# Kernel tuning notes

Hardware: AMD Instinct MI355X
Metric: run time of the kernel (lower is better)

## Reference

```python
import jax, jax.numpy as jnp
import numpy as np

N_NODES = 100000
N_EDGES = 1600000


def setup_inputs() -> dict:
    key = jax.random.key(0)
    ks = jax.random.split(key, 8)
    s = 0.1  # small init scale
    return {
        "x": jax.random.normal(ks[0], (N_NODES, 58), jnp.float32),
        "edge_index": jax.random.randint(ks[1], (2, N_EDGES), 0, N_NODES, dtype=jnp.int32),
        "Wi1": s * jax.random.normal(ks[2], (2, 58, 16), jnp.float32),
        "Wr1": s * jax.random.normal(ks[3], (2, 58, 16), jnp.float32),
        "b1": s * jax.random.normal(ks[4], (2, 16), jnp.float32),
        "Wi2": s * jax.random.normal(ks[5], (2, 16, 1), jnp.float32),
        "Wr2": s * jax.random.normal(ks[6], (2, 16, 1), jnp.float32),
        "b2": s * jax.random.normal(ks[7], (2, 1), jnp.float32),
    }


def _gcn_norm(edge_index, n_nodes):
    # PyG gcn_norm with add_self_loops=False: deg from target col, sym norm
    row, col = edge_index[0], edge_index[1]
    deg = jax.ops.segment_sum(jnp.ones((edge_index.shape[1],), jnp.float32), col,
                              num_segments=n_nodes)
    dis = jnp.where(deg > 0, jax.lax.rsqrt(jnp.maximum(deg, 1.0)), 0.0)
    return row, col, dis[row] * dis[col]  # per-edge norm


def _arma_layer(x, row, col, norm, Wi, Wr, b, n_nodes):
    # T=1, shared_weights, eval-mode (internal dropout off):
    # out_k = relu(A_hat @ (x @ Wi_k) + x @ Wr_k + b_k); mean over K stacks
    h = jnp.einsum('nf,kfo->kno', x, Wi)          # [K, N, F_out]
    msg = h[:, row, :] * norm[None, :, None]      # [K, E, F_out]
    agg = jax.vmap(lambda m: jax.ops.segment_sum(m, col, num_segments=n_nodes))(msg)
    root = jnp.einsum('nf,kfo->kno', x, Wr)       # [K, N, F_out]
    return jax.nn.relu(agg + root + b[:, None, :]).mean(axis=0)


def reference(x, edge_index, Wi1, Wr1, b1, Wi2, Wr2, b2):
    row, col, norm = _gcn_norm(edge_index, N_NODES)
    h = _arma_layer(x, row, col, norm, Wi1, Wr1, b1, N_NODES)  # conv1 (relu inside)
    h = jax.nn.relu(h)                                         # wrapper F.relu
    # F.dropout(p=0.5) is identity in eval mode
    out = _arma_layer(h, row, col, norm, Wi2, Wr2, b2, N_NODES)  # conv2
    return out  # [N, 1]
```

## Files before the change

kernel.cpp:

```cpp
#include <hip/hip_runtime.h>

#define NN 100000
#define NE 1600000

constexpr int F_IN = 58;
constexpr int FH2  = 32;
constexpr int KS   = 2;

constexpr int NB   = 391;
constexpr int NBLK = 256;
constexpr int EPB  = NE / NBLK;
constexpr int SCANN = NB * NBLK;
constexpr int SCAN_BLOCKS = (SCANN + 1023) / 1024;
constexpr int DN_NODES = 64;
constexpr int DENSE_BLOCKS = (NN + DN_NODES - 1) / DN_NODES;
constexpr int LROW = 136;

using short8 = __attribute__((ext_vector_type(8))) short;
using f32x4  = __attribute__((ext_vector_type(4))) float;

__device__ inline void splitbf(float v, short& hi, short& lo) {
    unsigned ub = __float_as_uint(v);
    unsigned short h = (unsigned short)(ub >> 16);
    float hif = __uint_as_float(((unsigned)h) << 16);
    float lof = v - hif;
    unsigned short l = (unsigned short)(__float_as_uint(lof) >> 16);
    hi = (short)h; lo = (short)l;
}

__device__ inline unsigned short bf16rne(float v) {
    unsigned u = __float_as_uint(v);
    unsigned r = u + 0x7FFF + ((u >> 16) & 1);
    return (unsigned short)(r >> 16);
}

__device__ inline float bf2f(unsigned short s) {
    return __uint_as_float(((unsigned)s) << 16);
}

__global__ void k_prep_w(const float* __restrict__ Wi, const float* __restrict__ Wr,
                         short* __restrict__ wpre) {
    int t = threadIdx.x;
    for (int idx = t; idx < 64 * 64; idx += 256) {
        int c = idx >> 6, i = idx & 63;
        int ko = c & 31, kst = ko >> 4, o = ko & 15;
        const float* W = (c < 32) ? Wi : Wr;
        float v = (i < F_IN) ? W[(kst * F_IN + i) * 16 + o] : 0.f;
        short hi, lo; splitbf(v, hi, lo);
        wpre[c * 128 + i] = hi;
        wpre[c * 128 + 64 + i] = lo;
    }
}

__global__ void k_hist_dense1(const int* __restrict__ col, int* __restrict__ bh,
                              const float* __restrict__ x,
                              const short* __restrict__ wpre,
                              const float* __restrict__ b,
                              unsigned short* __restrict__ h1b,
                              unsigned short* __restrict__ r1b) {
    __shared__ int hist[NB];
    __shared__ short sA[64 * LROW];
    __shared__ short sB[64 * LROW];
    int tid = threadIdx.x;

    if (blockIdx.x < NBLK) {
        int blk = blockIdx.x;
        for (int i = tid; i < NB; i += 256) hist[i] = 0;
        __syncthreads();
        const int2* c2p = (const int2*)&col[blk * EPB];
        for (int c = tid; c < EPB / 2; c += 256) {
            int2 cc = c2p[c];
            atomicAdd(&hist[cc.x >> 8], 1);
            atomicAdd(&hist[cc.y >> 8], 1);
        }
        __syncthreads();
        for (int i = tid; i < NB; i += 256)
            bh[i * NBLK + blk] = hist[i];
        return;
    }

    int nodeBase = (blockIdx.x - NBLK) * DN_NODES;
    for (int t = tid; t < 1024; t += 256) {
        int c = t >> 4, q8 = t & 15;
        *(short8*)&sB[c * LROW + q8 * 8] = *(const short8*)&wpre[c * 128 + q8 * 8];
    }
    for (int t = tid; t < 1024; t += 256) {
        int r = t >> 4, q4 = t & 15;
        int n = nodeBase + r;
        float v0 = 0.f, v1 = 0.f, v2 = 0.f, v3 = 0.f;
        int i0 = q4 * 4;
        if (n < NN && i0 < F_IN) {
            float2 a = *(const float2*)&x[(size_t)n * F_IN + i0];
            v0 = a.x; v1 = a.y;
            if (i0 + 2 < F_IN) {
                float2 c2 = *(const float2*)&x[(size_t)n * F_IN + i0 + 2];
                v2 = c2.x; v3 = c2.y;
            }
        }
        short h0, l0, h1s, l1s, h2s, l2s, h3s, l3s;
        splitbf(v0, h0, l0); splitbf(v1, h1s, l1s);
        splitbf(v2, h2s, l2s); splitbf(v3, h3s, l3s);
        *(short4*)&sA[r * LROW + q4 * 4]      = make_short4(h0, h1s, h2s, h3s);
        *(short4*)&sA[r * LROW + 64 + q4 * 4] = make_short4(l0, l1s, l2s, l3s);
    }
    __syncthreads();

    int lane = tid & 63, w = tid >> 6;
    int r15 = lane & 15, h4 = lane >> 4;
    const short* aB = &sA[(w * 16 + r15) * LROW];
    f32x4 acc0 = {0,0,0,0}, acc1 = {0,0,0,0}, acc2 = {0,0,0,0}, acc3 = {0,0,0,0};
    const int kaA[6] = {0, 32, 0, 32, 64, 96};
    const int kaB[6] = {0, 32, 64, 96, 0, 32};
#pragma unroll
    for (int s = 0; s < 6; s++) {
        short8 af = *(const short8*)&aB[kaA[s] + h4 * 8];
#define BMM(nt, accv) { \
        short8 bf = *(const short8*)&sB[(nt * 16 + r15) * LROW + kaB[s] + h4 * 8]; \
        accv = __builtin_amdgcn_mfma_f32_16x16x32_bf16(af, bf, accv, 0, 0, 0); }
        BMM(0, acc0) BMM(1, acc1) BMM(2, acc2) BMM(3, acc3)
#undef BMM
    }
    int nb0 = nodeBase + w * 16 + h4 * 4;
#define WH(nt, accv) { int colg = nt * 16 + r15; \
    if (nb0 + 0 < NN) h1b[(size_t)(nb0 + 0) * 32 + colg] = bf16rne(accv[0]); \
    if (nb0 + 1 < NN) h1b[(size_t)(nb0 + 1) * 32 + colg] = bf16rne(accv[1]); \
    if (nb0 + 2 < NN) h1b[(size_t)(nb0 + 2) * 32 + colg] = bf16rne(accv[2]); \
    if (nb0 + 3 < NN) h1b[(size_t)(nb0 + 3) * 32 + colg] = bf16rne(accv[3]); }
#define WR(nt, accv) { int colg = nt * 16 + r15 - 32; float bv = b[colg]; \
    if (nb0 + 0 < NN) r1b[(size_t)(nb0 + 0) * 32 + colg] = bf16rne(accv[0] + bv); \
    if (nb0 + 1 < NN) r1b[(size_t)(nb0 + 1) * 32 + colg] = bf16rne(accv[1] + bv); \
    if (nb0 + 2 < NN) r1b[(size_t)(nb0 + 2) * 32 + colg] = bf16rne(accv[2] + bv); \
    if (nb0 + 3 < NN) r1b[(size_t)(nb0 + 3) * 32 + colg] = bf16rne(accv[3] + bv); }
    WH(0, acc0) WH(1, acc1) WR(2, acc2) WR(3, acc3)
#undef WH
#undef WR
}

__global__ void k_scan1(int* __restrict__ bh, int* __restrict__ bsum) {
    __shared__ int ts[256];
    int tid = threadIdx.x;
    int base = blockIdx.x * 1024 + tid * 4;
    int v0 = (base + 0 < SCANN) ? bh[base + 0] : 0;
    int v1 = (base + 1 < SCANN) ? bh[base + 1] : 0;
    int v2 = (base + 2 < SCANN) ? bh[base + 2] : 0;
    int v3 = (base + 3 < SCANN) ? bh[base + 3] : 0;
    int p0 = v0, p1 = p0 + v1, p2 = p1 + v2, p3 = p2 + v3;
    ts[tid] = p3;
    __syncthreads();
    for (int off = 1; off < 256; off <<= 1) {
        int v = (tid >= off) ? ts[tid - off] : 0;
        __syncthreads();
        ts[tid] += v;
        __syncthreads();
    }
    int prev = (tid > 0) ? ts[tid - 1] : 0;
    if (base + 0 < SCANN) bh[base + 0] = prev + p0;
    if (base + 1 < SCANN) bh[base + 1] = prev + p1;
    if (base + 2 < SCANN) bh[base + 2] = prev + p2;
    if (base + 3 < SCANN) bh[base + 3] = prev + p3;
    if (tid == 255) bsum[blockIdx.x] = ts[255];
}

__global__ void k_scan2(const int* __restrict__ bsum, int* __restrict__ boff) {
    __shared__ int s[128];
    int tid = threadIdx.x;
    s[tid] = (tid < SCAN_BLOCKS) ? bsum[tid] : 0;
    __syncthreads();
    for (int off = 1; off < 128; off <<= 1) {
        int v = (tid >= off) ? s[tid - off] : 0;
        __syncthreads();
        s[tid] += v;
        __syncthreads();
    }
    if (tid < SCAN_BLOCKS) boff[tid] = (tid > 0) ? s[tid - 1] : 0;
}

__global__ void k_bscatter(const int* __restrict__ row, const int* __restrict__ col,
                           const int* __restrict__ bh, const int* __restrict__ boff,
                           int* __restrict__ ebuck) {
    __shared__ int cur[NB];
    int tid = threadIdx.x, blk = blockIdx.x;
    for (int i = tid; i < NB; i += 256) {
        int idx = i * NBLK + blk;
        cur[i] = (idx == 0) ? 0 : bh[idx - 1] + boff[(idx - 1) >> 10];
    }
    __syncthreads();
    int base = blk * EPB;
    const int2* c2p = (const int2*)&col[base];
    const int2* r2p = (const int2*)&row[base];
    for (int c = tid; c < EPB / 2; c += 256) {
        int2 cc = c2p[c];
        int2 rr = r2p[c];
        int p0 = atomicAdd(&cur[cc.x >> 8], 1);
        ebuck[p0] = (rr.x << 8) | (cc.x & 255);
        int p1 = atomicAdd(&cur[cc.y >> 8], 1);
        ebuck[p1] = (rr.y << 8) | (cc.y & 255);
    }
}

__global__ void __launch_bounds__(256) k_bcsr(const int* __restrict__ bh,
                                              const int* __restrict__ boff,
                                              const int* __restrict__ ebuck,
                                              int* __restrict__ inc, float* __restrict__ dis,
                                              int* __restrict__ esrc) {
    __shared__ int cnt[514];
    __shared__ int scn[256];
    __shared__ int cur[256];
    int b = blockIdx.x, tid = threadIdx.x;
    int i0 = b * NBLK - 1, i1 = (b + 1) * NBLK - 1;
    int start = (b == 0) ? 0 : bh[i0] + boff[i0 >> 10];
    int end   = bh[i1] + boff[i1 >> 10];
    cnt[tid] = 0; cnt[257 + tid] = 0;
    __syncthreads();
    int c0 = (tid & 1) * 257;
    for (int j = start + tid; j < end; j += 256)
        atomicAdd(&cnt[c0 + (ebuck[j] & 255)], 1);
    __syncthreads();
    int v = cnt[tid] + cnt[257 + tid];
    scn[tid] = v;
    __syncthreads();
    for (int off = 1; off < 256; off <<= 1) {
        int t = (tid >= off) ? scn[tid - off] : 0;
        __syncthreads();
        scn[tid] += t;
        __syncthreads();
    }
    int incl = scn[tid];
    cur[tid] = start + incl - v;
    int colIdx = (b << 8) + tid;
    if (colIdx < NN) {
        inc[colIdx] = start + incl;
        dis[colIdx] = (v > 0) ? rsqrtf((float)v) : 0.f;
    }
    __syncthreads();
    for (int j = start + tid; j < end; j += 256) {
        int e = ebuck[j];
        int pos = atomicAdd(&cur[e & 255], 1);
        esrc[pos] = e >> 8;
    }
}

__global__ void k_gather1_mid(const int* __restrict__ inc, const int* __restrict__ esrc,
                              const float* __restrict__ dis,
                              const unsigned short* __restrict__ h1b,
                              const unsigned short* __restrict__ r1b,
                              const float4* __restrict__ Wi2, const float4* __restrict__ Wr2,
                              const float* __restrict__ b2,
                              float* __restrict__ h2, float* __restrict__ r2) {
    int tid = blockIdx.x * blockDim.x + threadIdx.x;
    int n = tid >> 3, l = tid & 7;
    if (n >= NN) return;
    int js = (n == 0) ? 0 : inc[n - 1];
    int je = inc[n];
    float dn = dis[n];
    short4 rv4 = *(const short4*)&r1b[(size_t)n * 32 + l * 4];
    float4 acc;
    acc.x = bf2f((unsigned short)rv4.x);
    acc.y = bf2f((unsigned short)rv4.y);
    acc.z = bf2f((unsigned short)rv4.z);
    acc.w = bf2f((unsigned short)rv4.w);
    int j = js;
#define EDGE1(ss) { \
        float w = dis[ss] * dn; \
        short4 hv = *(const short4*)&h1b[(size_t)(ss) * 32 + l * 4]; \
        acc.x = fmaf(w, bf2f((unsigned short)hv.x), acc.x); \
        acc.y = fmaf(w, bf2f((unsigned short)hv.y), acc.y); \
        acc.z = fmaf(w, bf2f((unsigned short)hv.z), acc.z); \
        acc.w = fmaf(w, bf2f((unsigned short)hv.w), acc.w); }
    while (j < je && (j & 3)) { EDGE1(esrc[j]) j++; }
    for (; j + 3 < je; j += 4) {
        int4 s4 = *(const int4*)&esrc[j];
        EDGE1(s4.x) EDGE1(s4.y) EDGE1(s4.z) EDGE1(s4.w)
    }
    for (; j < je; j++) { EDGE1(esrc[j]) }
#undef EDGE1
    acc.x = fmaxf(acc.x, 0.f); acc.y = fmaxf(acc.y, 0.f);
    acc.z = fmaxf(acc.z, 0.f); acc.w = fmaxf(acc.w, 0.f);
    float4 h;
    h.x = 0.5f * (acc.x + __shfl_xor(acc.x, 4));
    h.y = 0.5f * (acc.y + __shfl_xor(acc.y, 4));
    h.z = 0.5f * (acc.z + __shfl_xor(acc.z, 4));
    h.w = 0.5f * (acc.w + __shfl_xor(acc.w, 4));
    float4 wi = Wi2[l], wr = Wr2[l];
    float p1 = h.x * wi.x + h.y * wi.y + h.z * wi.z + h.w * wi.w;
    float p2 = h.x * wr.x + h.y * wr.y + h.z * wr.z + h.w * wr.w;
    p1 += __shfl_xor(p1, 1); p1 += __shfl_xor(p1, 2);
    p2 += __shfl_xor(p2, 1); p2 += __shfl_xor(p2, 2);
    if ((l & 3) == 0) {
        int k = l >> 2;
        h2[n * 2 + k] = p1;
        r2[n * 2 + k] = p2 + b2[k];
    }
}

__global__ void k_gather2(const int* __restrict__ inc, const int* __restrict__ esrc,
                          const float* __restrict__ dis,
                          const float* __restrict__ h2, const float* __restrict__ r2,
                          float* __restrict__ out) {
    int tid = blockIdx.x * blockDim.x + threadIdx.x;
    int n = tid >> 3, l = tid & 7;
    if (n >= NN) return;
    int js = (n == 0) ? 0 : inc[n - 1];
    int je = inc[n];
    float dn = dis[n];
    float a0 = 0.f, a1v = 0.f;
    for (int j = js + l; j < je; j += 8) {
        int s = esrc[j];
        float w = dis[s] * dn;
        float2 hv = *(const float2*)&h2[(size_t)s * 2];
        a0  = fmaf(w, hv.x, a0);
        a1v = fmaf(w, hv.y, a1v);
    }
    a0  += __shfl_xor(a0, 1);  a0  += __shfl_xor(a0, 2);  a0  += __shfl_xor(a0, 4);
    a1v += __shfl_xor(a1v, 1); a1v += __shfl_xor(a1v, 2); a1v += __shfl_xor(a1v, 4);
    if (l == 0) {
        float2 rv = *(const float2*)&r2[(size_t)n * 2];
        out[n] = 0.5f * (fmaxf(a0 + rv.x, 0.f) + fmaxf(a1v + rv.y, 0.f));
    }
}

extern "C" void kernel_launch(void* const* d_in, const int* in_sizes, int n_in,
                              void* d_out, int out_size, void* d_ws, size_t ws_size,
                              hipStream_t stream) {
    const float* x   = (const float*)d_in[0];
    const int*   ei  = (const int*)d_in[1];
    const float* Wi1 = (const float*)d_in[2];
    const float* Wr1 = (const float*)d_in[3];
    const float* b1  = (const float*)d_in[4];
    const float* Wi2 = (const float*)d_in[5];
    const float* Wr2 = (const float*)d_in[6];
    const float* b2  = (const float*)d_in[7];
    float* out = (float*)d_out;

    const int* row = ei;
    const int* col = ei + NE;

    int*   bh    = (int*)d_ws;
    int*   bsum  = bh + SCANN;
    int*   boff  = bsum + 128;
    float* dis   = (float*)(boff + 128);
    int*   inc   = (int*)(dis + NN);
    short* wpre  = (short*)(inc + NN);
    int*   ebuck = (int*)(wpre + 8192);
    int*   esrc  = ebuck + NE;
    unsigned short* h1b = (unsigned short*)(esrc + NE);
    unsigned short* r1b = h1b + (size_t)NN * FH2;
    float* h2    = (float*)(r1b + (size_t)NN * FH2);
    float* r2    = h2 + (size_t)NN * KS;

    const int B = 256;
    k_prep_w<<<1, B, 0, stream>>>(Wi1, Wr1, wpre);
    k_hist_dense1<<<NBLK + DENSE_BLOCKS, B, 0, stream>>>(col, bh, x, wpre, b1, h1b, r1b);
    k_scan1<<<SCAN_BLOCKS, B, 0, stream>>>(bh, bsum);
    k_scan2<<<1, 128, 0, stream>>>(bsum, boff);
    k_bscatter<<<NBLK, B, 0, stream>>>(row, col, bh, boff, ebuck);
    k_bcsr<<<NB, B, 0, stream>>>(bh, boff, ebuck, inc, dis, esrc);
    k_gather1_mid<<<(NN * 8 + B - 1) / B, B, 0, stream>>>(inc, esrc, dis, h1b, r1b,
        (const float4*)Wi2, (const float4*)Wr2, b2, h2, r2);
    k_gather2<<<(NN * 8 + B - 1) / B, B, 0, stream>>>(inc, esrc, dis, h2, r2, out);
}
```

Measured before the change: 104.9 us.

## Merge CSR build kernels into one cooperative kernel and inline weight prep

```diff
diff --git a/kernel.cpp b/kernel.cpp
--- a/kernel.cpp
+++ b/kernel.cpp
@@ -1,4 +1,7 @@
 #include <hip/hip_runtime.h>
+#include <hip/hip_cooperative_groups.h>
+
+namespace cg = cooperative_groups;
 
 #define NN 100000
 #define NE 1600000
@@ -38,23 +41,9 @@
     return __uint_as_float(((unsigned)s) << 16);
 }
 
-__global__ void k_prep_w(const float* __restrict__ Wi, const float* __restrict__ Wr,
-                         short* __restrict__ wpre) {
-    int t = threadIdx.x;
-    for (int idx = t; idx < 64 * 64; idx += 256) {
-        int c = idx >> 6, i = idx & 63;
-        int ko = c & 31, kst = ko >> 4, o = ko & 15;
-        const float* W = (c < 32) ? Wi : Wr;
-        float v = (i < F_IN) ? W[(kst * F_IN + i) * 16 + o] : 0.f;
-        short hi, lo; splitbf(v, hi, lo);
-        wpre[c * 128 + i] = hi;
-        wpre[c * 128 + 64 + i] = lo;
-    }
-}
-
 __global__ void k_hist_dense1(const int* __restrict__ col, int* __restrict__ bh,
                               const float* __restrict__ x,
-                              const short* __restrict__ wpre,
+                              const float* __restrict__ Wi, const float* __restrict__ Wr,
                               const float* __restrict__ b,
                               unsigned short* __restrict__ h1b,
                               unsigned short* __restrict__ r1b) {
@@ -81,8 +70,20 @@
 
     int nodeBase = (blockIdx.x - NBLK) * DN_NODES;
     for (int t = tid; t < 1024; t += 256) {
-        int c = t >> 4, q8 = t & 15;
-        *(short8*)&sB[c * LROW + q8 * 8] = *(const short8*)&wpre[c * 128 + q8 * 8];
+        int c = t >> 4, q4 = t & 15;
+        int i0 = q4 * 4;
+        int ko = c & 31, kst = ko >> 4, o = ko & 15;
+        const float* W = (c < 32) ? Wi : Wr;
+        float v0 = 0.f, v1 = 0.f, v2 = 0.f, v3 = 0.f;
+        if (i0 + 0 < F_IN) v0 = W[(kst * F_IN + i0 + 0) * 16 + o];
+        if (i0 + 1 < F_IN) v1 = W[(kst * F_IN + i0 + 1) * 16 + o];
+        if (i0 + 2 < F_IN) v2 = W[(kst * F_IN + i0 + 2) * 16 + o];
+        if (i0 + 3 < F_IN) v3 = W[(kst * F_IN + i0 + 3) * 16 + o];
+        short h0, l0, h1s, l1s, h2s, l2s, h3s, l3s;
+        splitbf(v0, h0, l0); splitbf(v1, h1s, l1s);
+        splitbf(v2, h2s, l2s); splitbf(v3, h3s, l3s);
+        *(short4*)&sB[c * LROW + q4 * 4]      = make_short4(h0, h1s, h2s, h3s);
+        *(short4*)&sB[c * LROW + 64 + q4 * 4] = make_short4(l0, l1s, l2s, l3s);
     }
     for (int t = tid; t < 1024; t += 256) {
         int r = t >> 4, q4 = t & 15;
@@ -136,107 +137,115 @@
 #undef WR
 }
 
-__global__ void k_scan1(int* __restrict__ bh, int* __restrict__ bsum) {
-    __shared__ int ts[256];
-    int tid = threadIdx.x;
-    int base = blockIdx.x * 1024 + tid * 4;
-    int v0 = (base + 0 < SCANN) ? bh[base + 0] : 0;
-    int v1 = (base + 1 < SCANN) ? bh[base + 1] : 0;
-    int v2 = (base + 2 < SCANN) ? bh[base + 2] : 0;
-    int v3 = (base + 3 < SCANN) ? bh[base + 3] : 0;
-    int p0 = v0, p1 = p0 + v1, p2 = p1 + v2, p3 = p2 + v3;
-    ts[tid] = p3;
-    __syncthreads();
-    for (int off = 1; off < 256; off <<= 1) {
-        int v = (tid >= off) ? ts[tid - off] : 0;
-        __syncthreads();
-        ts[tid] += v;
-        __syncthreads();
-    }
-    int prev = (tid > 0) ? ts[tid - 1] : 0;
-    if (base + 0 < SCANN) bh[base + 0] = prev + p0;
-    if (base + 1 < SCANN) bh[base + 1] = prev + p1;
-    if (base + 2 < SCANN) bh[base + 2] = prev + p2;
-    if (base + 3 < SCANN) bh[base + 3] = prev + p3;
-    if (tid == 255) bsum[blockIdx.x] = ts[255];
-}
-
-__global__ void k_scan2(const int* __restrict__ bsum, int* __restrict__ boff) {
-    __shared__ int s[128];
-    int tid = threadIdx.x;
-    s[tid] = (tid < SCAN_BLOCKS) ? bsum[tid] : 0;
-    __syncthreads();
-    for (int off = 1; off < 128; off <<= 1) {
-        int v = (tid >= off) ? s[tid - off] : 0;
-        __syncthreads();
-        s[tid] += v;
-        __syncthreads();
-    }
-    if (tid < SCAN_BLOCKS) boff[tid] = (tid > 0) ? s[tid - 1] : 0;
-}
-
-__global__ void k_bscatter(const int* __restrict__ row, const int* __restrict__ col,
-                           const int* __restrict__ bh, const int* __restrict__ boff,
-                           int* __restrict__ ebuck) {
-    __shared__ int cur[NB];
-    int tid = threadIdx.x, blk = blockIdx.x;
-    for (int i = tid; i < NB; i += 256) {
-        int idx = i * NBLK + blk;
-        cur[i] = (idx == 0) ? 0 : bh[idx - 1] + boff[(idx - 1) >> 10];
-    }
-    __syncthreads();
-    int base = blk * EPB;
-    const int2* c2p = (const int2*)&col[base];
-    const int2* r2p = (const int2*)&row[base];
-    for (int c = tid; c < EPB / 2; c += 256) {
-        int2 cc = c2p[c];
-        int2 rr = r2p[c];
-        int p0 = atomicAdd(&cur[cc.x >> 8], 1);
-        ebuck[p0] = (rr.x << 8) | (cc.x & 255);
-        int p1 = atomicAdd(&cur[cc.y >> 8], 1);
-        ebuck[p1] = (rr.y << 8) | (cc.y & 255);
-    }
-}
-
-__global__ void __launch_bounds__(256) k_bcsr(const int* __restrict__ bh,
-                                              const int* __restrict__ boff,
-                                              const int* __restrict__ ebuck,
-                                              int* __restrict__ inc, float* __restrict__ dis,
-                                              int* __restrict__ esrc) {
-    __shared__ int cnt[514];
-    __shared__ int scn[256];
-    __shared__ int cur[256];
-    int b = blockIdx.x, tid = threadIdx.x;
-    int i0 = b * NBLK - 1, i1 = (b + 1) * NBLK - 1;
-    int start = (b == 0) ? 0 : bh[i0] + boff[i0 >> 10];
-    int end   = bh[i1] + boff[i1 >> 10];
-    cnt[tid] = 0; cnt[257 + tid] = 0;
-    __syncthreads();
-    int c0 = (tid & 1) * 257;
-    for (int j = start + tid; j < end; j += 256)
-        atomicAdd(&cnt[c0 + (ebuck[j] & 255)], 1);
-    __syncthreads();
-    int v = cnt[tid] + cnt[257 + tid];
-    scn[tid] = v;
-    __syncthreads();
-    for (int off = 1; off < 256; off <<= 1) {
-        int t = (tid >= off) ? scn[tid - off] : 0;
-        __syncthreads();
-        scn[tid] += t;
-        __syncthreads();
-    }
-    int incl = scn[tid];
-    cur[tid] = start + incl - v;
-    int colIdx = (b << 8) + tid;
-    if (colIdx < NN) {
-        inc[colIdx] = start + incl;
-        dis[colIdx] = (v > 0) ? rsqrtf((float)v) : 0.f;
-    }
-    __syncthreads();
-    for (int j = start + tid; j < end; j += 256) {
-        int e = ebuck[j];
-        int pos = atomicAdd(&cur[e & 255], 1);
-        esrc[pos] = e >> 8;
+__global__ void __launch_bounds__(256) k_csr(int* __restrict__ bh,
+                                             int* __restrict__ bsum,
+                                             int* __restrict__ boff,
+                                             const int* __restrict__ row,
+                                             const int* __restrict__ col,
+                                             int* __restrict__ ebuck,
+                                             int* __restrict__ inc,
+                                             float* __restrict__ dis,
+                                             int* __restrict__ esrc) {
+    cg::grid_group grid = cg::this_grid();
+    __shared__ int sh[1026];
+    int tid = threadIdx.x, b = blockIdx.x;
+
+    if (b < SCAN_BLOCKS) {
+        int* ts = sh;
+        int base = b * 1024 + tid * 4;
+        int v0 = (base + 0 < SCANN) ? bh[base + 0] : 0;
+        int v1 = (base + 1 < SCANN) ? bh[base + 1] : 0;
+        int v2 = (base + 2 < SCANN) ? bh[base + 2] : 0;
+        int v3 = (base + 3 < SCANN) ? bh[base + 3] : 0;
+        int p0 = v0, p1 = p0 + v1, p2 = p1 + v2, p3 = p2 + v3;
+        ts[tid] = p3;
+        __syncthreads();
+        for (int off = 1; off < 256; off <<= 1) {
+            int v = (tid >= off) ? ts[tid - off] : 0;
+            __syncthreads();
+            ts[tid] += v;
+            __syncthreads();
+        }
+        int prev = (tid > 0) ? ts[tid - 1] : 0;
+        if (base + 0 < SCANN) bh[base + 0] = prev + p0;
+        if (base + 1 < SCANN) bh[base + 1] = prev + p1;
+        if (base + 2 < SCANN) bh[base + 2] = prev + p2;
+        if (base + 3 < SCANN) bh[base + 3] = prev + p3;
+        if (tid == 255) bsum[b] = ts[255];
+    }
+    grid.sync();
+
+    if (b == 0) {
+        int* s = sh;
+        s[tid] = (tid < SCAN_BLOCKS) ? bsum[tid] : 0;
+        __syncthreads();
+        for (int off = 1; off < 256; off <<= 1) {
+            int v = (tid >= off) ? s[tid - off] : 0;
+            __syncthreads();
+            s[tid] += v;
+            __syncthreads();
+        }
+        if (tid < SCAN_BLOCKS) boff[tid] = (tid > 0) ? s[tid - 1] : 0;
+    }
+    grid.sync();
+
+    if (b < NBLK) {
+        int* cur = sh;
+        for (int i = tid; i < NB; i += 256) {
+            int idx = i * NBLK + b;
+            cur[i] = (idx == 0) ? 0 : bh[idx - 1] + boff[(idx - 1) >> 10];
+        }
+        __syncthreads();
+        int base = b * EPB;
+        const int2* c2p = (const int2*)&col[base];
+        const int2* r2p = (const int2*)&row[base];
+        for (int c = tid; c < EPB / 2; c += 256) {
+            int2 cc = c2p[c];
+            int2 rr = r2p[c];
+            int p0 = atomicAdd(&cur[cc.x >> 8], 1);
+            ebuck[p0] = (rr.x << 8) | (cc.x & 255);
+            int p1 = atomicAdd(&cur[cc.y >> 8], 1);
+            ebuck[p1] = (rr.y << 8) | (cc.y & 255);
+        }
+    }
+    grid.sync();
+
+    {
+        int* cnt = sh;
+        int* scn = sh + 514;
+        int* cur = sh + 770;
+        int i0 = b * NBLK - 1, i1 = (b + 1) * NBLK - 1;
+        int start = (b == 0) ? 0 : bh[i0] + boff[i0 >> 10];
+        int end   = bh[i1] + boff[i1 >> 10];
+        cnt[tid] = 0; cnt[257 + tid] = 0;
+        if (tid < 2) cnt[256 + tid * 257] = 0;
+        __syncthreads();
+        int c0 = (tid & 1) * 257;
+        for (int j = start + tid; j < end; j += 256)
+            atomicAdd(&cnt[c0 + (ebuck[j] & 255)], 1);
+        __syncthreads();
+        int v = cnt[tid] + cnt[257 + tid];
+        scn[tid] = v;
+        __syncthreads();
+        for (int off = 1; off < 256; off <<= 1) {
+            int t = (tid >= off) ? scn[tid - off] : 0;
+            __syncthreads();
+            scn[tid] += t;
+            __syncthreads();
+        }
+        int incl = scn[tid];
+        cur[tid] = start + incl - v;
+        int colIdx = (b << 8) + tid;
+        if (colIdx < NN) {
+            inc[colIdx] = start + incl;
+            dis[colIdx] = (v > 0) ? rsqrtf((float)v) : 0.f;
+        }
+        __syncthreads();
+        for (int j = start + tid; j < end; j += 256) {
+            int e = ebuck[j];
+            int pos = atomicAdd(&cur[e & 255], 1);
+            esrc[pos] = e >> 8;
+        }
     }
 }
 
@@ -340,8 +349,7 @@
     int*   boff  = bsum + 128;
     float* dis   = (float*)(boff + 128);
     int*   inc   = (int*)(dis + NN);
-    short* wpre  = (short*)(inc + NN);
-    int*   ebuck = (int*)(wpre + 8192);
+    int*   ebuck = inc + NN;
     int*   esrc  = ebuck + NE;
     unsigned short* h1b = (unsigned short*)(esrc + NE);
     unsigned short* r1b = h1b + (size_t)NN * FH2;
@@ -349,12 +357,13 @@
     float* r2    = h2 + (size_t)NN * KS;
 
     const int B = 256;
-    k_prep_w<<<1, B, 0, stream>>>(Wi1, Wr1, wpre);
-    k_hist_dense1<<<NBLK + DENSE_BLOCKS, B, 0, stream>>>(col, bh, x, wpre, b1, h1b, r1b);
-    k_scan1<<<SCAN_BLOCKS, B, 0, stream>>>(bh, bsum);
-    k_scan2<<<1, 128, 0, stream>>>(bsum, boff);
-    k_bscatter<<<NBLK, B, 0, stream>>>(row, col, bh, boff, ebuck);
-    k_bcsr<<<NB, B, 0, stream>>>(bh, boff, ebuck, inc, dis, esrc);
+    k_hist_dense1<<<NBLK + DENSE_BLOCKS, B, 0, stream>>>(col, bh, x, Wi1, Wr1, b1, h1b, r1b);
+    {
+        void* args[] = {(void*)&bh, (void*)&bsum, (void*)&boff, (void*)&row,
+                        (void*)&col, (void*)&ebuck, (void*)&inc, (void*)&dis,
+                        (void*)&esrc};
+        hipLaunchCooperativeKernel((void*)k_csr, dim3(NB), dim3(B), args, 0, stream);
+    }
     k_gather1_mid<<<(NN * 8 + B - 1) / B, B, 0, stream>>>(inc, esrc, dis, h1b, r1b,
         (const float4*)Wi2, (const float4*)Wr2, b2, h2, r2);
     k_gather2<<<(NN * 8 + B - 1) / B, B, 0, stream>>>(inc, esrc, dis, h2, r2, out);
```

Result: slower. 250.6 us (+139.0%).

## Fold weight prep and second scan into consumer kernels, drop two launches

Applied to the files above, without the earlier changes.

```diff
diff --git a/kernel.cpp b/kernel.cpp
--- a/kernel.cpp
+++ b/kernel.cpp
@@ -15,6 +15,7 @@
 constexpr int DN_NODES = 64;
 constexpr int DENSE_BLOCKS = (NN + DN_NODES - 1) / DN_NODES;
 constexpr int LROW = 136;
+constexpr int WELEM = KS * F_IN * 16;
 
 using short8 = __attribute__((ext_vector_type(8))) short;
 using f32x4  = __attribute__((ext_vector_type(4))) float;
@@ -38,23 +39,9 @@
     return __uint_as_float(((unsigned)s) << 16);
 }
 
-__global__ void k_prep_w(const float* __restrict__ Wi, const float* __restrict__ Wr,
-                         short* __restrict__ wpre) {
-    int t = threadIdx.x;
-    for (int idx = t; idx < 64 * 64; idx += 256) {
-        int c = idx >> 6, i = idx & 63;
-        int ko = c & 31, kst = ko >> 4, o = ko & 15;
-        const float* W = (c < 32) ? Wi : Wr;
-        float v = (i < F_IN) ? W[(kst * F_IN + i) * 16 + o] : 0.f;
-        short hi, lo; splitbf(v, hi, lo);
-        wpre[c * 128 + i] = hi;
-        wpre[c * 128 + 64 + i] = lo;
-    }
-}
-
 __global__ void k_hist_dense1(const int* __restrict__ col, int* __restrict__ bh,
                               const float* __restrict__ x,
-                              const short* __restrict__ wpre,
+                              const float* __restrict__ Wi, const float* __restrict__ Wr,
                               const float* __restrict__ b,
                               unsigned short* __restrict__ h1b,
                               unsigned short* __restrict__ r1b) {
@@ -80,9 +67,23 @@
     }
 
     int nodeBase = (blockIdx.x - NBLK) * DN_NODES;
-    for (int t = tid; t < 1024; t += 256) {
-        int c = t >> 4, q8 = t & 15;
-        *(short8*)&sB[c * LROW + q8 * 8] = *(const short8*)&wpre[c * 128 + q8 * 8];
+    for (int idx = tid; idx < WELEM; idx += 256) {
+        int kst = (idx >= F_IN * 16) ? 1 : 0;
+        int rem = idx - kst * (F_IN * 16);
+        int i = rem >> 4, o = rem & 15;
+        int c = kst * 16 + o;
+        short hi, lo;
+        splitbf(Wi[idx], hi, lo);
+        sB[c * LROW + i] = hi;
+        sB[c * LROW + 64 + i] = lo;
+        splitbf(Wr[idx], hi, lo);
+        sB[(c + 32) * LROW + i] = hi;
+        sB[(c + 32) * LROW + 64 + i] = lo;
+    }
+    for (int t = tid; t < 64 * 6; t += 256) {
+        int c = t / 6, i = 58 + (t - (t / 6) * 6);
+        sB[c * LROW + i] = 0;
+        sB[c * LROW + 64 + i] = 0;
     }
     for (int t = tid; t < 1024; t += 256) {
         int r = t >> 4, q4 = t & 15;
@@ -161,28 +162,27 @@
     if (tid == 255) bsum[blockIdx.x] = ts[255];
 }
 
-__global__ void k_scan2(const int* __restrict__ bsum, int* __restrict__ boff) {
-    __shared__ int s[128];
-    int tid = threadIdx.x;
-    s[tid] = (tid < SCAN_BLOCKS) ? bsum[tid] : 0;
-    __syncthreads();
-    for (int off = 1; off < 128; off <<= 1) {
-        int v = (tid >= off) ? s[tid - off] : 0;
-        __syncthreads();
-        s[tid] += v;
-        __syncthreads();
-    }
-    if (tid < SCAN_BLOCKS) boff[tid] = (tid > 0) ? s[tid - 1] : 0;
-}
+#define INLINE_BOFF(sb) \
+    if (tid < 128) sb[tid] = (tid < SCAN_BLOCKS) ? bsum[tid] : 0; \
+    __syncthreads(); \
+    for (int off = 1; off < 128; off <<= 1) { \
+        int t_ = (tid < 128 && tid >= off) ? sb[tid - off] : 0; \
+        __syncthreads(); \
+        if (tid < 128) sb[tid] += t_; \
+        __syncthreads(); \
+    }
+#define BOFF(sb, q) (((q) > 0) ? sb[(q) - 1] : 0)
 
 __global__ void k_bscatter(const int* __restrict__ row, const int* __restrict__ col,
-                           const int* __restrict__ bh, const int* __restrict__ boff,
+                           const int* __restrict__ bh, const int* __restrict__ bsum,
                            int* __restrict__ ebuck) {
     __shared__ int cur[NB];
+    __shared__ int sb[128];
     int tid = threadIdx.x, blk = blockIdx.x;
+    INLINE_BOFF(sb)
     for (int i = tid; i < NB; i += 256) {
         int idx = i * NBLK + blk;
-        cur[i] = (idx == 0) ? 0 : bh[idx - 1] + boff[(idx - 1) >> 10];
+        cur[i] = (idx == 0) ? 0 : bh[idx - 1] + BOFF(sb, (idx - 1) >> 10);
     }
     __syncthreads();
     int base = blk * EPB;
@@ -199,17 +199,19 @@
 }
 
 __global__ void __launch_bounds__(256) k_bcsr(const int* __restrict__ bh,
-                                              const int* __restrict__ boff,
+                                              const int* __restrict__ bsum,
                                               const int* __restrict__ ebuck,
                                               int* __restrict__ inc, float* __restrict__ dis,
                                               int* __restrict__ esrc) {
     __shared__ int cnt[514];
     __shared__ int scn[256];
     __shared__ int cur[256];
+    __shared__ int sb[128];
     int b = blockIdx.x, tid = threadIdx.x;
+    INLINE_BOFF(sb)
     int i0 = b * NBLK - 1, i1 = (b + 1) * NBLK - 1;
-    int start = (b == 0) ? 0 : bh[i0] + boff[i0 >> 10];
-    int end   = bh[i1] + boff[i1 >> 10];
+    int start = (b == 0) ? 0 : bh[i0] + BOFF(sb, i0 >> 10);
+    int end   = bh[i1] + BOFF(sb, i1 >> 10);
     cnt[tid] = 0; cnt[257 + tid] = 0;
     __syncthreads();
     int c0 = (tid & 1) * 257;
@@ -337,11 +339,9 @@
 
     int*   bh    = (int*)d_ws;
     int*   bsum  = bh + SCANN;
-    int*   boff  = bsum + 128;
-    float* dis   = (float*)(boff + 128);
+    float* dis   = (float*)(bsum + 128);
     int*   inc   = (int*)(dis + NN);
-    short* wpre  = (short*)(inc + NN);
-    int*   ebuck = (int*)(wpre + 8192);
+    int*   ebuck = inc + NN;
     int*   esrc  = ebuck + NE;
     unsigned short* h1b = (unsigned short*)(esrc + NE);
     unsigned short* r1b = h1b + (size_t)NN * FH2;
@@ -349,12 +349,10 @@
     float* r2    = h2 + (size_t)NN * KS;
 
     const int B = 256;
-    k_prep_w<<<1, B, 0, stream>>>(Wi1, Wr1, wpre);
-    k_hist_dense1<<<NBLK + DENSE_BLOCKS, B, 0, stream>>>(col, bh, x, wpre, b1, h1b, r1b);
+    k_hist_dense1<<<NBLK + DENSE_BLOCKS, B, 0, stream>>>(col, bh, x, Wi1, Wr1, b1, h1b, r1b);
     k_scan1<<<SCAN_BLOCKS, B, 0, stream>>>(bh, bsum);
-    k_scan2<<<1, 128, 0, stream>>>(bsum, boff);
-    k_bscatter<<<NBLK, B, 0, stream>>>(row, col, bh, boff, ebuck);
-    k_bcsr<<<NB, B, 0, stream>>>(bh, boff, ebuck, inc, dis, esrc);
+    k_bscatter<<<NBLK, B, 0, stream>>>(row, col, bh, bsum, ebuck);
+    k_bcsr<<<NB, B, 0, stream>>>(bh, bsum, ebuck, inc, dis, esrc);
     k_gather1_mid<<<(NN * 8 + B - 1) / B, B, 0, stream>>>(inc, esrc, dis, h1b, r1b,
         (const float4*)Wi2, (const float4*)Wr2, b2, h2, r2);
     k_gather2<<<(NN * 8 + B - 1) / B, B, 0, stream>>>(inc, esrc, dis, h2, r2, out);
```

Result: faster. 101.7 us (median of 2 runs) (-3.1%).
